# Performance work log

Hardware: AMD Instinct MI355X
Metric: run time of the kernel (lower is better)

Reference implementation:

```python
import jax, jax.numpy as jnp
import numpy as np

B, NB, DIM = 4096, 64, 256
CNT_R = 500
CNT_E = CNT_R * 2  # padding relation id == CNT_E maps to the masked row
N_WR = CNT_R * 2 + 1
N_ZQ = CNT_R * 2


def setup_inputs() -> dict:
    key = jax.random.key(0)
    ks = jax.random.split(key, 10)
    batch_nei_rid = jax.random.randint(ks[0], (B, NB), 0, N_WR, dtype=jnp.int64 if jax.config.read('jax_enable_x64') else jnp.int32)
    batch_nei_e_emb = jax.random.normal(ks[1], (B, NB, DIM), dtype=jnp.float32)
    batch_nei_rw = jax.random.uniform(ks[2], (B, NB), dtype=jnp.float32)
    batch_q_rid = jax.random.randint(ks[3], (B,), 0, N_ZQ, dtype=jnp.int32)
    # xavier-normal-ish params
    def xav(k, shape):
        fan_in, fan_out = shape[-1], shape[-2] if len(shape) > 1 else shape[-1]
        std = (2.0 / (fan_in + fan_out)) ** 0.5
        return (jax.random.normal(k, shape) * std).astype(jnp.float32)
    w_r_weight = xav(ks[4], (N_WR, DIM))
    zq_weight = xav(ks[5], (N_ZQ, DIM))
    attn_W_w = xav(ks[6], (2 * DIM, 2 * DIM))   # [out, in], torch Linear layout
    attn_W_b = jnp.zeros((2 * DIM,), jnp.float32)
    u_a_w = xav(ks[7], (1, 2 * DIM))
    u_a_b = jnp.zeros((1,), jnp.float32)
    return {
        'batch_nei_rid': batch_nei_rid,
        'batch_nei_e_emb': batch_nei_e_emb,
        'batch_nei_rw': batch_nei_rw,
        'batch_q_rid': batch_q_rid,
        'w_r_weight': w_r_weight,
        'zq_weight': zq_weight,
        'attn_W_w': attn_W_w,
        'attn_W_b': attn_W_b,
        'u_a_w': u_a_w,
        'u_a_b': u_a_b,
    }


def reference(batch_nei_rid, batch_nei_e_emb, batch_nei_rw, batch_q_rid,
              w_r_weight, zq_weight, attn_W_w, attn_W_b, u_a_w, u_a_b):
    # relation hyperplane gather + TransH-style projection
    w_r = w_r_weight[batch_nei_rid]                                   # [B,NB,D]
    nrm = jnp.maximum(jnp.linalg.norm(w_r, axis=-1, keepdims=True), 1e-12)
    wn = w_r / nrm                                                    # f.normalize(p=2)
    e_tr = batch_nei_e_emb - jnp.sum(batch_nei_e_emb * wn, axis=-1, keepdims=True) * wn
    # mask_emb: 1 for real rows, 0 for padding row (index CNT_E)
    mask = (batch_nei_rid < CNT_E).astype(e_tr.dtype)[..., None]
    e_tr = e_tr * mask
    # nn attention: concat(z_q, e_Tr) -> Linear -> tanh -> Linear(1)
    z_q = zq_weight[batch_q_rid][:, None, :]                          # [B,1,D]
    cat = jnp.concatenate([jnp.broadcast_to(z_q, e_tr.shape), e_tr], axis=-1)  # [B,NB,2D]
    h = jnp.tanh(jnp.einsum('bni,oi->bno', cat, attn_W_w) + attn_W_b)
    _alpha = jnp.einsum('bni,oi->bno', h, u_a_w)[..., 0] + u_a_b[0]   # [B,NB]
    # mask_weight: 1e19 at padding row, subtracted before softmax
    _alpha = _alpha - jnp.where(batch_nei_rid == CNT_E, jnp.asarray(1e19, _alpha.dtype), jnp.asarray(0.0, _alpha.dtype))
    alpha = jax.nn.softmax(_alpha, axis=-1)
    attn = alpha + batch_nei_rw                                       # use_logic_attention
    return jnp.sum(attn[..., None] * e_tr, axis=-2)                   # [B,D]
```

## Files before the change

kernel.cpp:

```cpp
#include <hip/hip_runtime.h>
#include <math.h>

#define NB    64
#define DIM   256
#define TWOD  512
#define CNTE  1000
#define E2S   264
#define LGS   17

typedef __attribute__((ext_vector_type(8))) short short8;
typedef __attribute__((ext_vector_type(4))) float f32x4;

union U16x8 { uint4 u; short8 s; };

__device__ __forceinline__ unsigned short f2bf(float x) {
    unsigned int u = __float_as_uint(x);
    u += 0x7fffu + ((u >> 16) & 1u);
    return (unsigned short)(u >> 16);
}
__device__ __forceinline__ float bf2f(unsigned short h) {
    return __uint_as_float(((unsigned int)h) << 16);
}
__device__ __forceinline__ float tanh_fast(float x) {
    float e = __expf(2.0f * x);
    return 1.0f - 2.0f / (e + 1.0f);
}

__global__ __launch_bounds__(256) void pack_w_kernel(
    const float* __restrict__ attn_W, unsigned short* __restrict__ wbf)
{
    int f = blockIdx.x * 256 + threadIdx.x;
    int j    = f & 7;
    int lane = (f >> 3) & 63;
    int kt   = (f >> 9) & 7;
    int ot   = f >> 12;
    int o = ot * 16 + (lane & 15);
    int k = kt * 32 + (lane >> 4) * 8 + j;
    wbf[f] = f2bf(attn_W[(size_t)o * TWOD + DIM + k]);
}

__global__ __launch_bounds__(256) void zpart_kernel(
    const float* __restrict__ zq_w, const float* __restrict__ attn_W,
    const float* __restrict__ attn_b, float* __restrict__ zp_all)
{
    __shared__ float zq[DIM];
    const int r = blockIdx.x, t = threadIdx.x;
    zq[t] = zq_w[(size_t)r * DIM + t];
    __syncthreads();
    #pragma unroll
    for (int oo = 0; oo < 2; ++oo) {
        int o = t + oo * 256;
        const float4* w4 = (const float4*)(attn_W + (size_t)o * TWOD);
        const float4* z4 = (const float4*)zq;
        float acc = attn_b[o];
        #pragma unroll 16
        for (int j = 0; j < 64; ++j) {
            float4 wv = w4[j], zv = z4[j];
            acc += wv.x * zv.x + wv.y * zv.y + wv.z * zv.z + wv.w * zv.w;
        }
        zp_all[(size_t)r * TWOD + o] = acc;
    }
}

__global__ __launch_bounds__(256, 2) void encoder_attn_kernel(
    const int*   __restrict__ nei_rid,
    const float* __restrict__ nei_e,
    const float* __restrict__ nei_rw,
    const int*   __restrict__ q_rid,
    const float* __restrict__ w_r,
    const float* __restrict__ u_a_w,
    const float* __restrict__ u_a_b,
    const unsigned short* __restrict__ wbf,
    const float* __restrict__ zp_all,
    float*       __restrict__ out)
{
    __shared__ __align__(16) unsigned short e2[NB * E2S];
    __shared__ float2 zpua[TWOD];
    __shared__ float  red_a[256];
    __shared__ float  red_b[256];
    __shared__ float  lgred[4 * NB * LGS];
    __shared__ float  pen[NB];
    __shared__ float  attn_lds[NB];

    const int b = blockIdx.x;
    const int t = threadIdx.x;

    const int qr = q_rid[b];
    zpua[t]       = make_float2(zp_all[(size_t)qr * TWOD + t],       u_a_w[t]);
    zpua[t + 256] = make_float2(zp_all[(size_t)qr * TWOD + t + 256], u_a_w[t + 256]);

    const int n = t >> 2, q = t & 3;
    const int rid = nei_rid[b * NB + n];
    const float4* e4 = (const float4*)(nei_e + ((size_t)(b * NB + n)) * DIM) + q * 16;
    const float4* w4 = (const float4*)(w_r + (size_t)rid * DIM) + q * 16;
    float sew = 0.f, sww = 0.f;
    #pragma unroll
    for (int j = 0; j < 16; ++j) {
        float4 ev = e4[j], wv = w4[j];
        sew += ev.x * wv.x + ev.y * wv.y + ev.z * wv.z + ev.w * wv.w;
        sww += wv.x * wv.x + wv.y * wv.y + wv.z * wv.z + wv.w * wv.w;
    }
    red_a[t] = sew;
    red_b[t] = sww;
    if (q == 0) pen[n] = (rid == CNTE) ? 1e19f : 0.f;
    __syncthreads();

    {
        float ew = red_a[n * 4] + red_a[n * 4 + 1] + red_a[n * 4 + 2] + red_a[n * 4 + 3];
        float ww = red_b[n * 4] + red_b[n * 4 + 1] + red_b[n * 4 + 2] + red_b[n * 4 + 3];
        float nc   = fmaxf(sqrtf(ww), 1e-12f);
        float coef = ew / (nc * nc);
        float maskf = (rid < CNTE) ? 1.f : 0.f;
        unsigned short* e2row = e2 + n * E2S + q * 64;
        #pragma unroll
        for (int jj = 0; jj < 8; ++jj) {
            float4 ev0 = e4[jj * 2],     wv0 = w4[jj * 2];
            float4 ev1 = e4[jj * 2 + 1], wv1 = w4[jj * 2 + 1];
            uint4 pk;
            pk.x = (unsigned int)f2bf((ev0.x - coef * wv0.x) * maskf)
                 | ((unsigned int)f2bf((ev0.y - coef * wv0.y) * maskf) << 16);
            pk.y = (unsigned int)f2bf((ev0.z - coef * wv0.z) * maskf)
                 | ((unsigned int)f2bf((ev0.w - coef * wv0.w) * maskf) << 16);
            pk.z = (unsigned int)f2bf((ev1.x - coef * wv1.x) * maskf)
                 | ((unsigned int)f2bf((ev1.y - coef * wv1.y) * maskf) << 16);
            pk.w = (unsigned int)f2bf((ev1.z - coef * wv1.z) * maskf)
                 | ((unsigned int)f2bf((ev1.w - coef * wv1.w) * maskf) << 16);
            *(uint4*)(e2row + jj * 8) = pk;
        }
    }
    __syncthreads();

    const int wv  = t >> 6;
    const int lane = t & 63;
    const int l15 = lane & 15, lq = lane >> 4;

    short8 afrag[4][8];
    #pragma unroll
    for (int mt = 0; mt < 4; ++mt)
        #pragma unroll
        for (int kt = 0; kt < 8; ++kt) {
            const unsigned short* p = e2 + (mt * 16 + l15) * E2S + kt * 32 + lq * 8;
            U16x8 u; u.u = *(const uint4*)p;
            afrag[mt][kt] = u.s;
        }

    f32x4 lpv[4];
    #pragma unroll
    for (int mt = 0; mt < 4; ++mt) lpv[mt] = (f32x4){0.f, 0.f, 0.f, 0.f};

    #pragma unroll 1
    for (int ot = 0; ot < 8; ++ot) {
        const int otg = wv * 8 + ot;
        short8 bfrag[8];
        #pragma unroll
        for (int kt = 0; kt < 8; ++kt) {
            U16x8 u; u.u = ((const uint4*)wbf)[(otg * 8 + kt) * 64 + lane];
            bfrag[kt] = u.s;
        }
        f32x4 acc[4];
        #pragma unroll
        for (int mt = 0; mt < 4; ++mt) acc[mt] = (f32x4){0.f, 0.f, 0.f, 0.f};
        #pragma unroll
        for (int kt = 0; kt < 8; ++kt)
            #pragma unroll
            for (int mt = 0; mt < 4; ++mt)
                acc[mt] = __builtin_amdgcn_mfma_f32_16x16x32_bf16(
                              afrag[mt][kt], bfrag[kt], acc[mt], 0, 0, 0);
        float2 zu = zpua[otg * 16 + l15];
        #pragma unroll
        for (int mt = 0; mt < 4; ++mt)
            #pragma unroll
            for (int r = 0; r < 4; ++r) {
                float h = tanh_fast(acc[mt][r] + zu.x);
                lpv[mt][r] += zu.y * h;
            }
    }
    #pragma unroll
    for (int mt = 0; mt < 4; ++mt)
        #pragma unroll
        for (int r = 0; r < 4; ++r) {
            int row = mt * 16 + lq * 4 + r;
            lgred[(wv * NB + row) * LGS + l15] = lpv[mt][r];
        }
    __syncthreads();

    {
        int nn = t & 63, wq = t >> 6;
        const float* lr = lgred + (wq * NB + nn) * LGS;
        float s = 0.f;
        #pragma unroll
        for (int i = 0; i < 16; ++i) s += lr[i];
        red_a[t] = s;
    }
    __syncthreads();

    if (t < NB) {
        float lgt = red_a[t] + red_a[64 + t] + red_a[128 + t] + red_a[192 + t]
                  + u_a_b[0] - pen[t];
        float m = lgt;
        #pragma unroll
        for (int off = 32; off > 0; off >>= 1) m = fmaxf(m, __shfl_xor(m, off));
        float ex = __expf(lgt - m);
        float s = ex;
        #pragma unroll
        for (int off = 32; off > 0; off >>= 1) s += __shfl_xor(s, off);
        attn_lds[t] = ex / s + nei_rw[b * NB + t];
    }
    __syncthreads();

    float oacc = 0.f;
    #pragma unroll 8
    for (int nn = 0; nn < NB; ++nn)
        oacc += attn_lds[nn] * bf2f(e2[nn * E2S + t]);
    out[(size_t)b * DIM + t] = oacc;
}

extern "C" void kernel_launch(void* const* d_in, const int* in_sizes, int n_in,
                              void* d_out, int out_size, void* d_ws, size_t ws_size,
                              hipStream_t stream) {
    const int*   nei_rid = (const int*)  d_in[0];
    const float* nei_e   = (const float*)d_in[1];
    const float* nei_rw  = (const float*)d_in[2];
    const int*   q_rid   = (const int*)  d_in[3];
    const float* w_r     = (const float*)d_in[4];
    const float* zq_w    = (const float*)d_in[5];
    const float* attn_W  = (const float*)d_in[6];
    const float* attn_b  = (const float*)d_in[7];
    const float* u_a_w   = (const float*)d_in[8];
    const float* u_a_b   = (const float*)d_in[9];
    float* out = (float*)d_out;

    const int B    = in_sizes[3];
    const int N_ZQ = in_sizes[5] / DIM;

    unsigned short* wbf    = (unsigned short*)d_ws;
    float*          zp_all = (float*)((char*)d_ws + 512 * 1024);

    hipLaunchKernelGGL(pack_w_kernel, dim3(512), dim3(256), 0, stream, attn_W, wbf);
    hipLaunchKernelGGL(zpart_kernel, dim3(N_ZQ), dim3(256), 0, stream,
                       zq_w, attn_W, attn_b, zp_all);
    hipLaunchKernelGGL(encoder_attn_kernel, dim3(B), dim3(256), 0, stream,
                       nei_rid, nei_e, nei_rw, q_rid, w_r,
                       u_a_w, u_a_b, wbf, zp_all, out);
}
```

Before: 625.6 us.

## Fuse z_q projection into attention kernel via MFMA and shuffle reductions

Drops the separate zpart kernel, which projected every zq row through the left half of attn_W. The packed bf16 weight now covers the full 512-wide input, and each block computes the z_q contribution with an extra MFMA chain seeded into the accumulators, adding the bias separately. Projection-coefficient reductions and logit row reductions now use wave shuffles instead of LDS round trips, and e/w values stay in registers rather than being reloaded. This costs extra MFMA work and B-fragment loads per block plus higher register pressure, and it quantizes z_q to bf16.

```diff
diff --git a/kernel.cpp b/kernel.cpp
--- a/kernel.cpp
+++ b/kernel.cpp
@@ -6,7 +6,6 @@
 #define TWOD  512
 #define CNTE  1000
 #define E2S   264
-#define LGS   17
 
 typedef __attribute__((ext_vector_type(8))) short short8;
 typedef __attribute__((ext_vector_type(4))) float f32x4;
@@ -32,34 +31,11 @@
     int f = blockIdx.x * 256 + threadIdx.x;
     int j    = f & 7;
     int lane = (f >> 3) & 63;
-    int kt   = (f >> 9) & 7;
-    int ot   = f >> 12;
+    int kt   = (f >> 9) & 15;
+    int ot   = f >> 13;
     int o = ot * 16 + (lane & 15);
     int k = kt * 32 + (lane >> 4) * 8 + j;
-    wbf[f] = f2bf(attn_W[(size_t)o * TWOD + DIM + k]);
-}
-
-__global__ __launch_bounds__(256) void zpart_kernel(
-    const float* __restrict__ zq_w, const float* __restrict__ attn_W,
-    const float* __restrict__ attn_b, float* __restrict__ zp_all)
-{
-    __shared__ float zq[DIM];
-    const int r = blockIdx.x, t = threadIdx.x;
-    zq[t] = zq_w[(size_t)r * DIM + t];
-    __syncthreads();
-    #pragma unroll
-    for (int oo = 0; oo < 2; ++oo) {
-        int o = t + oo * 256;
-        const float4* w4 = (const float4*)(attn_W + (size_t)o * TWOD);
-        const float4* z4 = (const float4*)zq;
-        float acc = attn_b[o];
-        #pragma unroll 16
-        for (int j = 0; j < 64; ++j) {
-            float4 wv = w4[j], zv = z4[j];
-            acc += wv.x * zv.x + wv.y * zv.y + wv.z * zv.z + wv.w * zv.w;
-        }
-        zp_all[(size_t)r * TWOD + o] = acc;
-    }
+    wbf[f] = f2bf(attn_W[(size_t)o * TWOD + k]);
 }
 
 __global__ __launch_bounds__(256, 2) void encoder_attn_kernel(
@@ -68,17 +44,17 @@
     const float* __restrict__ nei_rw,
     const int*   __restrict__ q_rid,
     const float* __restrict__ w_r,
+    const float* __restrict__ zq_w,
+    const float* __restrict__ attn_b,
     const float* __restrict__ u_a_w,
     const float* __restrict__ u_a_b,
     const unsigned short* __restrict__ wbf,
-    const float* __restrict__ zp_all,
     float*       __restrict__ out)
 {
     __shared__ __align__(16) unsigned short e2[NB * E2S];
-    __shared__ float2 zpua[TWOD];
+    __shared__ __align__(16) unsigned short zq2[DIM];
+    __shared__ float2 bua[TWOD];
     __shared__ float  red_a[256];
-    __shared__ float  red_b[256];
-    __shared__ float  lgred[4 * NB * LGS];
     __shared__ float  pen[NB];
     __shared__ float  attn_lds[NB];
 
@@ -86,52 +62,50 @@
     const int t = threadIdx.x;
 
     const int qr = q_rid[b];
-    zpua[t]       = make_float2(zp_all[(size_t)qr * TWOD + t],       u_a_w[t]);
-    zpua[t + 256] = make_float2(zp_all[(size_t)qr * TWOD + t + 256], u_a_w[t + 256]);
+    bua[t]       = make_float2(attn_b[t],       u_a_w[t]);
+    bua[t + 256] = make_float2(attn_b[t + 256], u_a_w[t + 256]);
+    zq2[t] = f2bf(zq_w[(size_t)qr * DIM + t]);
 
     const int n = t >> 2, q = t & 3;
     const int rid = nei_rid[b * NB + n];
     const float4* e4 = (const float4*)(nei_e + ((size_t)(b * NB + n)) * DIM) + q * 16;
     const float4* w4 = (const float4*)(w_r + (size_t)rid * DIM) + q * 16;
-    float sew = 0.f, sww = 0.f;
-    #pragma unroll
-    for (int j = 0; j < 16; ++j) {
-        float4 ev = e4[j], wv = w4[j];
-        sew += ev.x * wv.x + ev.y * wv.y + ev.z * wv.z + ev.w * wv.w;
-        sww += wv.x * wv.x + wv.y * wv.y + wv.z * wv.z + wv.w * wv.w;
-    }
-    red_a[t] = sew;
-    red_b[t] = sww;
-    if (q == 0) pen[n] = (rid == CNTE) ? 1e19f : 0.f;
-    __syncthreads();
-
     {
-        float ew = red_a[n * 4] + red_a[n * 4 + 1] + red_a[n * 4 + 2] + red_a[n * 4 + 3];
-        float ww = red_b[n * 4] + red_b[n * 4 + 1] + red_b[n * 4 + 2] + red_b[n * 4 + 3];
-        float nc   = fmaxf(sqrtf(ww), 1e-12f);
-        float coef = ew / (nc * nc);
+        float4 ev[16], wv[16];
+        float sew = 0.f, sww = 0.f;
+        #pragma unroll
+        for (int j = 0; j < 16; ++j) {
+            ev[j] = e4[j]; wv[j] = w4[j];
+            sew += ev[j].x * wv[j].x + ev[j].y * wv[j].y + ev[j].z * wv[j].z + ev[j].w * wv[j].w;
+            sww += wv[j].x * wv[j].x + wv[j].y * wv[j].y + wv[j].z * wv[j].z + wv[j].w * wv[j].w;
+        }
+        sew += __shfl_xor(sew, 1); sew += __shfl_xor(sew, 2);
+        sww += __shfl_xor(sww, 1); sww += __shfl_xor(sww, 2);
+        float nc   = fmaxf(sqrtf(sww), 1e-12f);
+        float coef = sew / (nc * nc);
         float maskf = (rid < CNTE) ? 1.f : 0.f;
+        if (q == 0) pen[n] = (rid == CNTE) ? 1e19f : 0.f;
         unsigned short* e2row = e2 + n * E2S + q * 64;
         #pragma unroll
         for (int jj = 0; jj < 8; ++jj) {
-            float4 ev0 = e4[jj * 2],     wv0 = w4[jj * 2];
-            float4 ev1 = e4[jj * 2 + 1], wv1 = w4[jj * 2 + 1];
+            float4 e0 = ev[jj * 2],     w0 = wv[jj * 2];
+            float4 e1 = ev[jj * 2 + 1], w1 = wv[jj * 2 + 1];
             uint4 pk;
-            pk.x = (unsigned int)f2bf((ev0.x - coef * wv0.x) * maskf)
-                 | ((unsigned int)f2bf((ev0.y - coef * wv0.y) * maskf) << 16);
-            pk.y = (unsigned int)f2bf((ev0.z - coef * wv0.z) * maskf)
-                 | ((unsigned int)f2bf((ev0.w - coef * wv0.w) * maskf) << 16);
-            pk.z = (unsigned int)f2bf((ev1.x - coef * wv1.x) * maskf)
-                 | ((unsigned int)f2bf((ev1.y - coef * wv1.y) * maskf) << 16);
-            pk.w = (unsigned int)f2bf((ev1.z - coef * wv1.z) * maskf)
-                 | ((unsigned int)f2bf((ev1.w - coef * wv1.w) * maskf) << 16);
+            pk.x = (unsigned int)f2bf((e0.x - coef * w0.x) * maskf)
+                 | ((unsigned int)f2bf((e0.y - coef * w0.y) * maskf) << 16);
+            pk.y = (unsigned int)f2bf((e0.z - coef * w0.z) * maskf)
+                 | ((unsigned int)f2bf((e0.w - coef * w0.w) * maskf) << 16);
+            pk.z = (unsigned int)f2bf((e1.x - coef * w1.x) * maskf)
+                 | ((unsigned int)f2bf((e1.y - coef * w1.y) * maskf) << 16);
+            pk.w = (unsigned int)f2bf((e1.z - coef * w1.z) * maskf)
+                 | ((unsigned int)f2bf((e1.w - coef * w1.w) * maskf) << 16);
             *(uint4*)(e2row + jj * 8) = pk;
         }
     }
     __syncthreads();
 
-    const int wv  = t >> 6;
-    const int lane = t & 63;
+    const int wv_id = t >> 6;
+    const int lane  = t & 63;
     const int l15 = lane & 15, lq = lane >> 4;
 
     short8 afrag[4][8];
@@ -150,23 +124,31 @@
 
     #pragma unroll 1
     for (int ot = 0; ot < 8; ++ot) {
-        const int otg = wv * 8 + ot;
-        short8 bfrag[8];
+        const int otg = wv_id * 8 + ot;
+        const uint4* wp = (const uint4*)wbf + (size_t)(otg * 16) * 64 + lane;
+        short8 bz[8], be[8];
+        #pragma unroll
+        for (int kt = 0; kt < 8; ++kt) { U16x8 u; u.u = wp[kt * 64]; bz[kt] = u.s; }
+        #pragma unroll
+        for (int kt = 0; kt < 8; ++kt) { U16x8 u; u.u = wp[(kt + 8) * 64]; be[kt] = u.s; }
+
+        f32x4 accz = (f32x4){0.f, 0.f, 0.f, 0.f};
         #pragma unroll
         for (int kt = 0; kt < 8; ++kt) {
-            U16x8 u; u.u = ((const uint4*)wbf)[(otg * 8 + kt) * 64 + lane];
-            bfrag[kt] = u.s;
+            U16x8 u; u.u = *(const uint4*)(zq2 + kt * 32 + lq * 8);
+            accz = __builtin_amdgcn_mfma_f32_16x16x32_bf16(u.s, bz[kt], accz, 0, 0, 0);
         }
         f32x4 acc[4];
         #pragma unroll
-        for (int mt = 0; mt < 4; ++mt) acc[mt] = (f32x4){0.f, 0.f, 0.f, 0.f};
+        for (int mt = 0; mt < 4; ++mt) acc[mt] = accz;
         #pragma unroll
         for (int kt = 0; kt < 8; ++kt)
             #pragma unroll
             for (int mt = 0; mt < 4; ++mt)
                 acc[mt] = __builtin_amdgcn_mfma_f32_16x16x32_bf16(
-                              afrag[mt][kt], bfrag[kt], acc[mt], 0, 0, 0);
-        float2 zu = zpua[otg * 16 + l15];
+                              afrag[mt][kt], be[kt], acc[mt], 0, 0, 0);
+
+        float2 zu = bua[otg * 16 + l15];
         #pragma unroll
         for (int mt = 0; mt < 4; ++mt)
             #pragma unroll
@@ -175,23 +157,16 @@
                 lpv[mt][r] += zu.y * h;
             }
     }
+
     #pragma unroll
     for (int mt = 0; mt < 4; ++mt)
         #pragma unroll
         for (int r = 0; r < 4; ++r) {
-            int row = mt * 16 + lq * 4 + r;
-            lgred[(wv * NB + row) * LGS + l15] = lpv[mt][r];
-        }
-    __syncthreads();
-
-    {
-        int nn = t & 63, wq = t >> 6;
-        const float* lr = lgred + (wq * NB + nn) * LGS;
-        float s = 0.f;
-        #pragma unroll
-        for (int i = 0; i < 16; ++i) s += lr[i];
-        red_a[t] = s;
-    }
+            float v = lpv[mt][r];
+            v += __shfl_xor(v, 1); v += __shfl_xor(v, 2);
+            v += __shfl_xor(v, 4); v += __shfl_xor(v, 8);
+            if (l15 == 0) red_a[wv_id * 64 + mt * 16 + lq * 4 + r] = v;
+        }
     __syncthreads();
 
     if (t < NB) {
@@ -230,16 +205,12 @@
     const float* u_a_b   = (const float*)d_in[9];
     float* out = (float*)d_out;
 
-    const int B    = in_sizes[3];
-    const int N_ZQ = in_sizes[5] / DIM;
-
-    unsigned short* wbf    = (unsigned short*)d_ws;
-    float*          zp_all = (float*)((char*)d_ws + 512 * 1024);
-
-    hipLaunchKernelGGL(pack_w_kernel, dim3(512), dim3(256), 0, stream, attn_W, wbf);
-    hipLaunchKernelGGL(zpart_kernel, dim3(N_ZQ), dim3(256), 0, stream,
-                       zq_w, attn_W, attn_b, zp_all);
+    const int B = in_sizes[3];
+
+    unsigned short* wbf = (unsigned short*)d_ws;
+
+    hipLaunchKernelGGL(pack_w_kernel, dim3(1024), dim3(256), 0, stream, attn_W, wbf);
     hipLaunchKernelGGL(encoder_attn_kernel, dim3(B), dim3(256), 0, stream,
-                       nei_rid, nei_e, nei_rw, q_rid, w_r,
-                       u_a_w, u_a_b, wbf, zp_all, out);
-}
+                       nei_rid, nei_e, nei_rw, q_rid, w_r, zq_w,
+                       attn_b, u_a_w, u_a_b, wbf, out);
+}
```

Result: faster. 525.4 us (-16.0%).
